# Kernel tuning notes

Hardware: AMD Instinct MI355X
Metric: run time of the kernel (lower is better)

Reference implementation:

```python
import jax, jax.numpy as jnp
import numpy as np

B, T, S, SYM, FFT = 256, 4, 2, 14, 128   # batch, num_tx, streams_per_tx, ofdm symbols, fft size
NSC, GUARD = 108, 10                      # effective subcarriers, guard offset
L = SYM * NSC                             # 1512, de-mash matrix dimension


def setup_inputs() -> dict:
    key = jax.random.key(0)
    k1, k2, k3, k4 = jax.random.split(key, 4)
    scale = 1.0 / np.sqrt(L).astype(np.float32)  # keep C roughly unitary-scaled
    return {
        "x_real": jax.random.normal(k1, (B, T, S, SYM, FFT), jnp.float32),
        "x_imag": jax.random.normal(k2, (B, T, S, SYM, FFT), jnp.float32),
        "C_real": jax.random.normal(k3, (L, L), jnp.float32) * scale,
        "C_imag": jax.random.normal(k4, (L, L), jnp.float32) * scale,
        "sc_ind": jnp.arange(NSC, dtype=jnp.int32) + GUARD,  # effective subcarrier indices
    }


def reference(x_real, x_imag, C_real, C_imag, sc_ind):
    # Complex RG and de-mash matrix
    x = jax.lax.complex(x_real, x_imag)           # [B,T,S,SYM,FFT] complex64
    C = jax.lax.complex(C_real, C_imag)           # [L,L] complex64

    # gather effective subcarriers along last axis
    y = jnp.take(x, sc_ind, axis=-1)              # [B,T,S,SYM,NSC]
    b, t, s, sym, nsc = y.shape

    # flatten_last_dims(y, 2) and multiply from right by C^H (adjoint=True)
    yf = y.reshape(b, t, s, sym * nsc)            # [B,T,S,L]
    yf = jnp.einsum('btsl,ml->btsm', yf, jnp.conj(C))  # y @ C^H
    y = yf.reshape(b, t, s, sym, nsc)             # [B,T,S,SYM,NSC]

    # scatter back into the full grid (equivalent to the transpose/scatter_nd/transpose chain,
    # since sc_ind is unique and the scatter is along the subcarrier axis)
    out = jnp.zeros(x.shape, x.dtype).at[..., sc_ind].set(y)

    # return real/imag stacked so the output is a single float32 array
    return jnp.stack([out.real, out.imag], axis=0)  # [2,B,T,S,SYM,FFT]
```

## Files before the change

### kernel.cpp

```cpp
#include <hip/hip_runtime.h>
#include <cstdint>
#include <cstddef>


typedef _Float16 half_t;
typedef half_t half8 __attribute__((ext_vector_type(8)));
typedef half_t half4 __attribute__((ext_vector_type(4)));
typedef half_t half2_t __attribute__((ext_vector_type(2)));
typedef float floatx4 __attribute__((ext_vector_type(4)));
typedef float floatv4 __attribute__((ext_vector_type(4)));

#define M_DIM 2048
#define N_DIM 3072
#define K_DIM 3072
#define LDIM 1512
#define NSC 108
#define SYMS 14
#define FFT 128
#define ROWLEN (SYMS * FFT)

#define BM 64
#define BN 128
#define BK 128
#define NITER (K_DIM / BK)

#define PA2_BLOCKS 6048
#define PW2_BLOCKS 9072
#define PAP_BLOCKS 48
#define PG_BLOCKS 4480
#define PREP_BLOCKS (PA2_BLOCKS + PW2_BLOCKS + PAP_BLOCKS + PG_BLOCKS)

typedef __attribute__((address_space(3))) uint32_t lds_u32_t;
typedef const __attribute__((address_space(1))) uint32_t glob_u32_t;

__device__ __forceinline__ void gl2lds16(const void* g, void* l) {
    __builtin_amdgcn_global_load_lds((glob_u32_t*)g, (lds_u32_t*)l, 16, 0, 0);
}

__global__ __launch_bounds__(256) void prep_all(
    const float* __restrict__ xr, const float* __restrict__ xi,
    const float* __restrict__ Cr, const float* __restrict__ Ci,
    const int* __restrict__ sc,
    half_t* __restrict__ A, half_t* __restrict__ W, float* __restrict__ out)
{
    const int b = blockIdx.x;
    const int t = threadIdx.x;

    if (b < PA2_BLOCKS) {
        int idx = b * 256 + t;
        int jp = idx % 54;
        int rest = idx / 54;
        int sym = rest % 14;
        int row = rest / 14;
        int s0 = sc[2 * jp];
        int s1 = sc[2 * jp + 1];
        const float* xrp = xr + (size_t)row * ROWLEN + sym * FFT;
        const float* xip = xi + (size_t)row * ROWLEN + sym * FFT;
        half2_t hr = { (half_t)xrp[s0], (half_t)xrp[s1] };
        half2_t hi = { (half_t)xip[s0], (half_t)xip[s1] };
        size_t dst = (size_t)row * K_DIM + sym * NSC + 2 * jp;
        *(half2_t*)(A + dst) = hr;
        *(half2_t*)(A + dst + LDIM) = hi;
    } else if (b < PA2_BLOCKS + PW2_BLOCKS) {
        int idx = (b - PA2_BLOCKS) * 256 + t;
        int kq = idx % 756;
        int n = idx / 756;
        int k0 = kq * 4;
        floatv4 f = {0.0f, 0.0f, 0.0f, 0.0f};
        if (n < LDIM) {
            if (k0 < LDIM)
                f = *(const floatv4*)(Cr + (size_t)n * LDIM + k0);
            else
                f = *(const floatv4*)(Ci + (size_t)n * LDIM + (k0 - LDIM));
        } else if (n < 2 * LDIM) {
            int m = n - LDIM;
            if (k0 < LDIM) {
                f = *(const floatv4*)(Ci + (size_t)m * LDIM + k0);
                f = -f;
            } else {
                f = *(const floatv4*)(Cr + (size_t)m * LDIM + (k0 - LDIM));
            }
        }
        half4 h = { (half_t)f.x, (half_t)f.y, (half_t)f.z, (half_t)f.w };
        *(half4*)(W + (size_t)n * K_DIM + k0) = h;
    } else if (b < PA2_BLOCKS + PW2_BLOCKS + PAP_BLOCKS) {
        int idx = (b - PA2_BLOCKS - PW2_BLOCKS) * 256 + t;
        int c = idx % 6;
        int row = idx / 6;
        half8 z = {};
        *(half8*)(A + (size_t)row * K_DIM + 2 * LDIM + c * 8) = z;
    } else {
        int idx = (b - PA2_BLOCKS - PW2_BLOCKS - PAP_BLOCKS) * 256 + t;
        int c20 = idx % 20;
        int rest = idx / 20;
        int sym = rest % 14;
        int rowri = rest / 14;
        int col = (c20 < 10) ? c20 : (NSC + c20);
        out[(size_t)rowri * ROWLEN + sym * FFT + col] = 0.0f;
    }
}

__global__ __launch_bounds__(256) void gemm_scatter(
    const half_t* __restrict__ A,
    const half_t* __restrict__ W,
    const int* __restrict__ sc,
    float* __restrict__ out)
{
    __shared__ __align__(16) half_t As[BM * BK];
    __shared__ __align__(16) half_t Bs[BN * BK];

    const int t = threadIdx.x;
    const int bn = blockIdx.x;
    const int bm = blockIdx.y;
    const int lane = t & 63;
    const int wn = (t >> 6) * 32;

    floatx4 acc[4][2] = {};

    const half_t* gAp[4];
    const half_t* gBp[8];
    half_t* lAp[4];
    half_t* lBp[8];
#pragma unroll
    for (int r = 0; r < 4; ++r) {
        int c = r * 256 + t;
        int row = c >> 4, slot = c & 15;
        int g = slot ^ (row & 15);
        gAp[r] = A + (size_t)(bm * BM + row) * K_DIM + g * 8;
        lAp[r] = As + c * 8;
    }
#pragma unroll
    for (int r = 0; r < 8; ++r) {
        int c = r * 256 + t;
        int row = c >> 4, slot = c & 15;
        int g = slot ^ (row & 15);
        gBp[r] = W + (size_t)(bn * BN + row) * K_DIM + g * 8;
        lBp[r] = Bs + c * 8;
    }

    const int fr = lane & 15;
    const int cr = lane >> 4;

    for (int kb = 0; kb < NITER; ++kb) {
        __syncthreads();
#pragma unroll
        for (int r = 0; r < 4; ++r) gl2lds16(gAp[r], lAp[r]);
#pragma unroll
        for (int r = 0; r < 8; ++r) gl2lds16(gBp[r], lBp[r]);
#pragma unroll
        for (int r = 0; r < 4; ++r) gAp[r] += BK;
#pragma unroll
        for (int r = 0; r < 8; ++r) gBp[r] += BK;
        __syncthreads();

#pragma unroll
        for (int h = 0; h < 2; ++h) {
            half8 af[2][4], bf[2][2];
#pragma unroll
            for (int ss = 0; ss < 2; ++ss) {
                int slot = ((h << 3) | (ss << 2) | cr) ^ fr;
#pragma unroll
                for (int i = 0; i < 4; ++i)
                    af[ss][i] = *(const half8*)&As[(i * 16 + fr) * BK + slot * 8];
#pragma unroll
                for (int j = 0; j < 2; ++j)
                    bf[ss][j] = *(const half8*)&Bs[(wn + j * 16 + fr) * BK + slot * 8];
            }
#pragma unroll
            for (int ss = 0; ss < 2; ++ss)
#pragma unroll
                for (int i = 0; i < 4; ++i)
#pragma unroll
                    for (int j = 0; j < 2; ++j)
                        acc[i][j] = __builtin_amdgcn_mfma_f32_16x16x32_f16(
                            af[ss][i], bf[ss][j], acc[i][j], 0, 0, 0);
        }
    }

    const int col_base = bn * BN + wn + (lane & 15);
    const int row_base = bm * BM + ((lane >> 4) * 4);
#pragma unroll
    for (int j = 0; j < 2; ++j) {
        int n = col_base + j * 16;
        if (n >= 2 * LDIM) continue;
        int ri = (n >= LDIM) ? 1 : 0;
        int nn = n - ri * LDIM;
        int sym = nn / NSC;
        int jj = nn - sym * NSC;
        size_t colOff = (size_t)ri * (M_DIM * ROWLEN) + sym * FFT + sc[jj];
#pragma unroll
        for (int i = 0; i < 4; ++i) {
            int row0 = row_base + i * 16;
#pragma unroll
            for (int r = 0; r < 4; ++r) {
                out[colOff + (size_t)(row0 + r) * ROWLEN] = acc[i][j][r];
            }
        }
    }
}

extern "C" void kernel_launch(void* const* d_in, const int* in_sizes, int n_in,
                              void* d_out, int out_size, void* d_ws, size_t ws_size,
                              hipStream_t stream) {
    const float* xr = (const float*)d_in[0];
    const float* xi = (const float*)d_in[1];
    const float* Cr = (const float*)d_in[2];
    const float* Ci = (const float*)d_in[3];
    const int* sc   = (const int*)d_in[4];
    float* out = (float*)d_out;

    half_t* Ah = (half_t*)d_ws;
    half_t* Wh = (half_t*)((char*)d_ws + (size_t)M_DIM * K_DIM * 2);

    prep_all<<<PREP_BLOCKS, 256, 0, stream>>>(
        xr, xi, Cr, Ci, sc, Ah, Wh, out);

    dim3 grid(N_DIM / BN, M_DIM / BM);
    gemm_scatter<<<grid, 256, 0, stream>>>(Ah, Wh, sc, out);
}
```

Before: 158.0 us.

## Compute complex GEMM with four real products instead of a doubled real-embedded weight

Replaces the 2L x 2L real embedding of the complex matrix with a half-size W holding [Cr | Ci] per row. Each K tile loads the real and imaginary halves of A and W, and four MFMA accumulators (RR, II, IR, RI) are combined at writeback into the real and imaginary outputs. The GEMM N dimension drops from 3072 to 1536, so the W conversion work and W bytes are halved while the MFMA count stays the same. Tiles change to 64x64x64 with a 2x2 wave layout and a launch-bounds occupancy hint, at the cost of more accumulator registers and more scattered stores per thread.

```diff
diff --git a/kernel.cpp b/kernel.cpp
--- a/kernel.cpp
+++ b/kernel.cpp
@@ -11,8 +11,9 @@
 typedef float floatv4 __attribute__((ext_vector_type(4)));
 
 #define M_DIM 2048
-#define N_DIM 3072
 #define K_DIM 3072
+#define L_PAD 1536
+#define N2_DIM 1536
 #define LDIM 1512
 #define NSC 108
 #define SYMS 14
@@ -20,12 +21,12 @@
 #define ROWLEN (SYMS * FFT)
 
 #define BM 64
-#define BN 128
-#define BK 128
-#define NITER (K_DIM / BK)
+#define BN 64
+#define BK 64
+#define NITER (L_PAD / BK)
 
 #define PA2_BLOCKS 6048
-#define PW2_BLOCKS 9072
+#define PW2_BLOCKS 4608
 #define PAP_BLOCKS 48
 #define PG_BLOCKS 4480
 #define PREP_BLOCKS (PA2_BLOCKS + PW2_BLOCKS + PAP_BLOCKS + PG_BLOCKS)
@@ -60,25 +61,21 @@
         half2_t hi = { (half_t)xip[s0], (half_t)xip[s1] };
         size_t dst = (size_t)row * K_DIM + sym * NSC + 2 * jp;
         *(half2_t*)(A + dst) = hr;
-        *(half2_t*)(A + dst + LDIM) = hi;
+        *(half2_t*)(A + dst + L_PAD) = hi;
     } else if (b < PA2_BLOCKS + PW2_BLOCKS) {
         int idx = (b - PA2_BLOCKS) * 256 + t;
-        int kq = idx % 756;
-        int n = idx / 756;
+        int kq = idx % 768;
+        int n = idx / 768;
         int k0 = kq * 4;
         floatv4 f = {0.0f, 0.0f, 0.0f, 0.0f};
         if (n < LDIM) {
-            if (k0 < LDIM)
-                f = *(const floatv4*)(Cr + (size_t)n * LDIM + k0);
-            else
-                f = *(const floatv4*)(Ci + (size_t)n * LDIM + (k0 - LDIM));
-        } else if (n < 2 * LDIM) {
-            int m = n - LDIM;
-            if (k0 < LDIM) {
-                f = *(const floatv4*)(Ci + (size_t)m * LDIM + k0);
-                f = -f;
+            if (k0 < L_PAD) {
+                if (k0 < LDIM)
+                    f = *(const floatv4*)(Cr + (size_t)n * LDIM + k0);
             } else {
-                f = *(const floatv4*)(Cr + (size_t)m * LDIM + (k0 - LDIM));
+                int l = k0 - L_PAD;
+                if (l < LDIM)
+                    f = *(const floatv4*)(Ci + (size_t)n * LDIM + l);
             }
         }
         half4 h = { (half_t)f.x, (half_t)f.y, (half_t)f.z, (half_t)f.w };
@@ -87,8 +84,9 @@
         int idx = (b - PA2_BLOCKS - PW2_BLOCKS) * 256 + t;
         int c = idx % 6;
         int row = idx / 6;
+        int col = (c < 3) ? (LDIM + c * 8) : (L_PAD + LDIM + (c - 3) * 8);
         half8 z = {};
-        *(half8*)(A + (size_t)row * K_DIM + 2 * LDIM + c * 8) = z;
+        *(half8*)(A + (size_t)row * K_DIM + col) = z;
     } else {
         int idx = (b - PA2_BLOCKS - PW2_BLOCKS - PAP_BLOCKS) * 256 + t;
         int c20 = idx % 20;
@@ -100,42 +98,39 @@
     }
 }
 
-__global__ __launch_bounds__(256) void gemm_scatter(
+__global__ __launch_bounds__(256, 3) void gemm_scatter(
     const half_t* __restrict__ A,
     const half_t* __restrict__ W,
     const int* __restrict__ sc,
     float* __restrict__ out)
 {
-    __shared__ __align__(16) half_t As[BM * BK];
-    __shared__ __align__(16) half_t Bs[BN * BK];
+    __shared__ __align__(16) half_t As[BM * 2 * BK];
+    __shared__ __align__(16) half_t Ws[BN * 2 * BK];
 
     const int t = threadIdx.x;
     const int bn = blockIdx.x;
     const int bm = blockIdx.y;
     const int lane = t & 63;
-    const int wn = (t >> 6) * 32;
-
-    floatx4 acc[4][2] = {};
-
-    const half_t* gAp[4];
-    const half_t* gBp[8];
-    half_t* lAp[4];
-    half_t* lBp[8];
+    const int w = t >> 6;
+    const int wm = (w >> 1) * 32;
+    const int wn = (w & 1) * 32;
+
+    floatx4 aRR[2][2] = {}, aII[2][2] = {}, aIR[2][2] = {}, aRI[2][2] = {};
+
+    const half_t* gA[4];
+    const half_t* gW[4];
+    half_t* lA[4];
+    half_t* lW[4];
 #pragma unroll
     for (int r = 0; r < 4; ++r) {
         int c = r * 256 + t;
         int row = c >> 4, slot = c & 15;
         int g = slot ^ (row & 15);
-        gAp[r] = A + (size_t)(bm * BM + row) * K_DIM + g * 8;
-        lAp[r] = As + c * 8;
-    }
-#pragma unroll
-    for (int r = 0; r < 8; ++r) {
-        int c = r * 256 + t;
-        int row = c >> 4, slot = c & 15;
-        int g = slot ^ (row & 15);
-        gBp[r] = W + (size_t)(bn * BN + row) * K_DIM + g * 8;
-        lBp[r] = Bs + c * 8;
+        int gcol = (g < 8) ? g * 8 : (L_PAD + (g - 8) * 8);
+        gA[r] = A + (size_t)(bm * BM + row) * K_DIM + gcol;
+        lA[r] = As + c * 8;
+        gW[r] = W + (size_t)(bn * BN + row) * K_DIM + gcol;
+        lW[r] = Ws + c * 8;
     }
 
     const int fr = lane & 15;
@@ -144,56 +139,64 @@
     for (int kb = 0; kb < NITER; ++kb) {
         __syncthreads();
 #pragma unroll
-        for (int r = 0; r < 4; ++r) gl2lds16(gAp[r], lAp[r]);
-#pragma unroll
-        for (int r = 0; r < 8; ++r) gl2lds16(gBp[r], lBp[r]);
-#pragma unroll
-        for (int r = 0; r < 4; ++r) gAp[r] += BK;
-#pragma unroll
-        for (int r = 0; r < 8; ++r) gBp[r] += BK;
+        for (int r = 0; r < 4; ++r) gl2lds16(gA[r], lA[r]);
+#pragma unroll
+        for (int r = 0; r < 4; ++r) gl2lds16(gW[r], lW[r]);
+#pragma unroll
+        for (int r = 0; r < 4; ++r) { gA[r] += BK; gW[r] += BK; }
         __syncthreads();
 
 #pragma unroll
-        for (int h = 0; h < 2; ++h) {
-            half8 af[2][4], bf[2][2];
-#pragma unroll
-            for (int ss = 0; ss < 2; ++ss) {
-                int slot = ((h << 3) | (ss << 2) | cr) ^ fr;
-#pragma unroll
-                for (int i = 0; i < 4; ++i)
-                    af[ss][i] = *(const half8*)&As[(i * 16 + fr) * BK + slot * 8];
-#pragma unroll
-                for (int j = 0; j < 2; ++j)
-                    bf[ss][j] = *(const half8*)&Bs[(wn + j * 16 + fr) * BK + slot * 8];
-            }
-#pragma unroll
-            for (int ss = 0; ss < 2; ++ss)
-#pragma unroll
-                for (int i = 0; i < 4; ++i)
-#pragma unroll
-                    for (int j = 0; j < 2; ++j)
-                        acc[i][j] = __builtin_amdgcn_mfma_f32_16x16x32_f16(
-                            af[ss][i], bf[ss][j], acc[i][j], 0, 0, 0);
+        for (int ss = 0; ss < 2; ++ss) {
+            const int sR = ((ss * 4 + cr) ^ fr) * 8;
+            const int sI = ((8 + ss * 4 + cr) ^ fr) * 8;
+            half8 yr[2], yi[2], cR[2], cI[2];
+#pragma unroll
+            for (int i = 0; i < 2; ++i) {
+                int rb = (wm + i * 16 + fr) * (2 * BK);
+                yr[i] = *(const half8*)&As[rb + sR];
+                yi[i] = *(const half8*)&As[rb + sI];
+            }
+#pragma unroll
+            for (int j = 0; j < 2; ++j) {
+                int rb = (wn + j * 16 + fr) * (2 * BK);
+                cR[j] = *(const half8*)&Ws[rb + sR];
+                cI[j] = *(const half8*)&Ws[rb + sI];
+            }
+#pragma unroll
+            for (int i = 0; i < 2; ++i)
+#pragma unroll
+                for (int j = 0; j < 2; ++j) {
+                    aRR[i][j] = __builtin_amdgcn_mfma_f32_16x16x32_f16(
+                        yr[i], cR[j], aRR[i][j], 0, 0, 0);
+                    aII[i][j] = __builtin_amdgcn_mfma_f32_16x16x32_f16(
+                        yi[i], cI[j], aII[i][j], 0, 0, 0);
+                    aIR[i][j] = __builtin_amdgcn_mfma_f32_16x16x32_f16(
+                        yi[i], cR[j], aIR[i][j], 0, 0, 0);
+                    aRI[i][j] = __builtin_amdgcn_mfma_f32_16x16x32_f16(
+                        yr[i], cI[j], aRI[i][j], 0, 0, 0);
+                }
         }
     }
 
-    const int col_base = bn * BN + wn + (lane & 15);
-    const int row_base = bm * BM + ((lane >> 4) * 4);
+    const int rq = lane >> 4;
 #pragma unroll
     for (int j = 0; j < 2; ++j) {
-        int n = col_base + j * 16;
-        if (n >= 2 * LDIM) continue;
-        int ri = (n >= LDIM) ? 1 : 0;
-        int nn = n - ri * LDIM;
-        int sym = nn / NSC;
-        int jj = nn - sym * NSC;
-        size_t colOff = (size_t)ri * (M_DIM * ROWLEN) + sym * FFT + sc[jj];
-#pragma unroll
-        for (int i = 0; i < 4; ++i) {
-            int row0 = row_base + i * 16;
+        int n = bn * BN + wn + j * 16 + fr;
+        if (n >= LDIM) continue;
+        int sym = n / NSC;
+        int jj = n - sym * NSC;
+        size_t colR = (size_t)sym * FFT + sc[jj];
+        size_t colI = (size_t)M_DIM * ROWLEN + colR;
+#pragma unroll
+        for (int i = 0; i < 2; ++i) {
+            int m0 = bm * BM + wm + i * 16 + rq * 4;
 #pragma unroll
             for (int r = 0; r < 4; ++r) {
-                out[colOff + (size_t)(row0 + r) * ROWLEN] = acc[i][j][r];
+                float vr = aRR[i][j][r] + aII[i][j][r];
+                float vi = aIR[i][j][r] - aRI[i][j][r];
+                out[colR + (size_t)(m0 + r) * ROWLEN] = vr;
+                out[colI + (size_t)(m0 + r) * ROWLEN] = vi;
             }
         }
     }
@@ -215,6 +218,6 @@
     prep_all<<<PREP_BLOCKS, 256, 0, stream>>>(
         xr, xi, Cr, Ci, sc, Ah, Wh, out);
 
-    dim3 grid(N_DIM / BN, M_DIM / BM);
+    dim3 grid(N2_DIM / BN, M_DIM / BM);
     gemm_scatter<<<grid, 256, 0, stream>>>(Ah, Wh, sc, out);
 }
```

Result: faster. 144.7 us (-8.5%).
